# Optimization experiments

Measured on AMD Instinct MI355X. Metric: run time of the kernel, lower is better.

The kernel has to match this reference:

```python
import jax, jax.numpy as jnp
import numpy as np

B, N, F_IN, D = 32768, 4, 512, 64  # N fixed to 4 by the max_pool(4,1)+reshape


def setup_inputs() -> dict:
    key = jax.random.key(0)
    k1, k2, k3, k4 = jax.random.split(key, 4)
    scale = 1.0 / np.sqrt(F_IN)
    return {
        "drug": jax.random.normal(k1, (B, N, F_IN), dtype=jnp.float32),
        "Wk": jax.random.normal(k2, (F_IN, D), dtype=jnp.float32) * scale,
        "Wq": jax.random.normal(k3, (F_IN, D), dtype=jnp.float32) * scale,
        "Wv": jax.random.normal(k4, (F_IN, D), dtype=jnp.float32) * scale,
    }


def reference(drug, Wk, Wq, Wv):
    # projections: torch nn.Linear(bias=False) -> x @ W  (W stored as [in, out] here)
    k = jnp.einsum("bnf,fd->bnd", drug, Wk)
    q = jnp.einsum("bnf,fd->bnd", drug, Wq)
    v = jnp.einsum("bnf,fd->bnd", drug, Wv)
    # score = bmm(K, Q^T); NOTE: no 1/sqrt(d) scaling, matching the source
    score = jnp.einsum("bnd,bmd->bnm", k, q)  # [B, N, N]
    attn = jax.nn.softmax(score, axis=2)
    out = jnp.einsum("bnm,bmd->bnd", attn, v)  # [B, N, D]
    # max_pool2d kernel (4,1), stride (4,1) over N=4 -> max over axis 1, then reshape [B, D]
    return jnp.max(out, axis=1)
```

## Files before the change

### kernel.cpp

```cpp
#include <hip/hip_runtime.h>
#include <hip/hip_fp16.h>

#define BTOT   32768
#define FIN    512
#define NCOLS  192
#define KSTEPS 16
#define NTILES 12
#define WH_ELEMS (KSTEPS * NTILES * 64 * 8)
#define CHUNK_HALVES (NTILES * 64 * 8)
#define CHUNK_BYTES  (CHUNK_HALVES * 2)

using half8   = __attribute__((ext_vector_type(8))) _Float16;
using floatx4 = __attribute__((ext_vector_type(4))) float;

#define GLOAD_LDS16(gp, lp)                                                  \
    __builtin_amdgcn_global_load_lds(                                        \
        (const __attribute__((address_space(1))) void*)(gp),                 \
        (__attribute__((address_space(3))) void*)(lp), 16, 0, 0)

__global__ void convert_w_kernel(const float* __restrict__ Wk,
                                 const float* __restrict__ Wq,
                                 const float* __restrict__ Wv,
                                 _Float16* __restrict__ Wh) {
    int idx = blockIdx.x * blockDim.x + threadIdx.x;
    if (idx >= WH_ELEMS) return;
    int j    = idx & 7;
    int lane = (idx >> 3) & 63;
    int t    = (idx >> 9) % NTILES;
    int kk   = idx / CHUNK_HALVES;
    int k = kk * 32 + (lane >> 4) * 8 + j;
    int n = t * 16 + (lane & 15);
    const float* src = (n < 64) ? Wk : (n < 128) ? Wq : Wv;
    Wh[idx] = (_Float16)src[k * 64 + (n & 63)];
}

__global__ __launch_bounds__(256) void attn_fused_kernel(
        const float* __restrict__ drug,
        const _Float16* __restrict__ Wh,
        float* __restrict__ out)
{
    __shared__ __align__(16) char lds[2 * CHUNK_BYTES];

    const int tid  = threadIdx.x;
    const int wave = tid >> 6;
    const int lane = tid & 63;
    const int quad = lane >> 4;
    const int l15  = lane & 15;

    const int row = blockIdx.x * 64 + wave * 16 + l15;
    const float* arow = drug + (size_t)row * FIN + quad * 8;
    const char* gW = (const char*)Wh;

    floatx4 acc[NTILES];
#pragma unroll
    for (int t = 0; t < NTILES; ++t) acc[t] = (floatx4){0.f, 0.f, 0.f, 0.f};

#define STAGE(K)                                                             \
    do {                                                                     \
        const char* _s = gW + (size_t)(K) * CHUNK_BYTES;                     \
        char* _d = lds + ((K) & 1) * CHUNK_BYTES;                            \
        _Pragma("unroll")                                                    \
        for (int _i = 0; _i < 3; ++_i) {                                     \
            const int _off = (wave + 4 * _i) * 1024;                         \
            GLOAD_LDS16(_s + _off + lane * 16, _d + _off);                   \
        }                                                                    \
    } while (0)

    STAGE(0);
    float4 a0 = ((const float4*)arow)[0];
    float4 a1 = ((const float4*)arow)[1];
    STAGE(1);

#pragma unroll
    for (int k = 0; k < KSTEPS; ++k) {
        if (k < KSTEPS - 1)
            asm volatile("s_waitcnt vmcnt(3)" ::: "memory");
        else
            asm volatile("s_waitcnt vmcnt(0)" ::: "memory");
        asm volatile("" ::: "memory");
        __builtin_amdgcn_s_barrier();
        asm volatile("" ::: "memory");

        float4 n0, n1;
        if (k < KSTEPS - 1) {
            const float4* ap = (const float4*)(arow + (k + 1) * 32);
            n0 = ap[0];
            n1 = ap[1];
        }

        half8 af;
        af[0] = (_Float16)a0.x; af[1] = (_Float16)a0.y;
        af[2] = (_Float16)a0.z; af[3] = (_Float16)a0.w;
        af[4] = (_Float16)a1.x; af[5] = (_Float16)a1.y;
        af[6] = (_Float16)a1.z; af[7] = (_Float16)a1.w;

        const _Float16* lh = (const _Float16*)(lds + (k & 1) * CHUNK_BYTES);
#pragma unroll
        for (int t = 0; t < NTILES; ++t) {
            half8 bf = *((const half8*)(lh + (t * 64 + lane) * 8));
            acc[t] = __builtin_amdgcn_mfma_f32_16x16x32_f16(af, bf, acc[t], 0, 0, 0);
        }

        if (k < KSTEPS - 2) {
            asm volatile("" ::: "memory");
            __builtin_amdgcn_s_barrier();
            asm volatile("" ::: "memory");
            STAGE(k + 2);
        }
        a0 = n0; a1 = n1;
    }
#undef STAGE

    float p[4][4];
#pragma unroll
    for (int n = 0; n < 4; ++n)
#pragma unroll
        for (int m = 0; m < 4; ++m) {
            float s = 0.f;
#pragma unroll
            for (int t = 0; t < 4; ++t) s += acc[t][n] * acc[4 + t][m];
            p[n][m] = s;
        }

#pragma unroll
    for (int mask = 1; mask < 16; mask <<= 1) {
#pragma unroll
        for (int n = 0; n < 4; ++n)
#pragma unroll
            for (int m = 0; m < 4; ++m)
                p[n][m] += __shfl_xor(p[n][m], mask, 64);
    }

    float res[4] = {-INFINITY, -INFINITY, -INFINITY, -INFINITY};
#pragma unroll
    for (int n = 0; n < 4; ++n) {
        float mx = fmaxf(fmaxf(p[n][0], p[n][1]), fmaxf(p[n][2], p[n][3]));
        float e0 = __expf(p[n][0] - mx);
        float e1 = __expf(p[n][1] - mx);
        float e2 = __expf(p[n][2] - mx);
        float e3 = __expf(p[n][3] - mx);
        float inv = 1.f / (e0 + e1 + e2 + e3);
#pragma unroll
        for (int t = 0; t < 4; ++t) {
            float o = (e0 * acc[8 + t][0] + e1 * acc[8 + t][1] +
                       e2 * acc[8 + t][2] + e3 * acc[8 + t][3]) * inv;
            res[t] = fmaxf(res[t], o);
        }
    }

    const int b = blockIdx.x * 16 + wave * 4 + quad;
#pragma unroll
    for (int t = 0; t < 4; ++t)
        out[b * 64 + t * 16 + l15] = res[t];
}

extern "C" void kernel_launch(void* const* d_in, const int* in_sizes, int n_in,
                              void* d_out, int out_size, void* d_ws, size_t ws_size,
                              hipStream_t stream) {
    const float* drug = (const float*)d_in[0];
    const float* Wk   = (const float*)d_in[1];
    const float* Wq   = (const float*)d_in[2];
    const float* Wv   = (const float*)d_in[3];
    float* out = (float*)d_out;
    _Float16* Wh = (_Float16*)d_ws;

    convert_w_kernel<<<(WH_ELEMS + 255) / 256, 256, 0, stream>>>(Wk, Wq, Wv, Wh);
    attn_fused_kernel<<<BTOT / 16, 256, 0, stream>>>(drug, Wh, out);
}
```

Baseline: 372.0 us.

## Keep full K/Q weights resident in LDS, stream V from global, persistent row tiles

Splits the converted fp16 weights into a K/Q section and a separate V section. Each 512-thread block loads the whole K/Q weight matrix (128 KB) into LDS once, then loops over four 128-row tiles, so the per-k-step double-buffered staging and its barriers go away. V weight fragments are read straight from global/L2 into registers with a one-step prefetch. This cuts repeated weight staging and synchronisation, at the cost of large LDS use (one block per CU), fewer blocks, and extra register pressure from the prefetched V fragments.

After: 708.2 us. +90.4%, slower.

```diff
diff --git a/kernel.cpp b/kernel.cpp
--- a/kernel.cpp
+++ b/kernel.cpp
@@ -3,12 +3,16 @@
 
 #define BTOT   32768
 #define FIN    512
-#define NCOLS  192
 #define KSTEPS 16
 #define NTILES 12
 #define WH_ELEMS (KSTEPS * NTILES * 64 * 8)
 #define CHUNK_HALVES (NTILES * 64 * 8)
-#define CHUNK_BYTES  (CHUNK_HALVES * 2)
+#define KQ_HALVES (KSTEPS * 8 * 512)
+#define KQ_BYTES  (KQ_HALVES * 2)
+#define WAVES  8
+#define ROWTILES 4
+#define ROWS_PER_BLOCK (WAVES * 16 * ROWTILES)
+#define NBLOCKS (BTOT * 4 / ROWS_PER_BLOCK)
 
 using half8   = __attribute__((ext_vector_type(8))) _Float16;
 using floatx4 = __attribute__((ext_vector_type(4))) float;
@@ -31,15 +35,19 @@
     int k = kk * 32 + (lane >> 4) * 8 + j;
     int n = t * 16 + (lane & 15);
     const float* src = (n < 64) ? Wk : (n < 128) ? Wq : Wv;
-    Wh[idx] = (_Float16)src[k * 64 + (n & 63)];
+    _Float16 val = (_Float16)src[k * 64 + (n & 63)];
+    size_t dst = (t < 8)
+        ? ((size_t)(kk * 8 + t) * 512 + lane * 8 + j)
+        : (size_t)KQ_HALVES + ((size_t)(kk * 4 + (t - 8)) * 512 + lane * 8 + j);
+    Wh[dst] = val;
 }
 
-__global__ __launch_bounds__(256) void attn_fused_kernel(
+__global__ __launch_bounds__(512) void attn_fused_kernel(
         const float* __restrict__ drug,
         const _Float16* __restrict__ Wh,
         float* __restrict__ out)
 {
-    __shared__ __align__(16) char lds[2 * CHUNK_BYTES];
+    extern __shared__ __align__(16) char lds[];
 
     const int tid  = threadIdx.x;
     const int wave = tid >> 6;
@@ -47,111 +55,114 @@
     const int quad = lane >> 4;
     const int l15  = lane & 15;
 
-    const int row = blockIdx.x * 64 + wave * 16 + l15;
-    const float* arow = drug + (size_t)row * FIN + quad * 8;
-    const char* gW = (const char*)Wh;
+    {
+        const char* gk = (const char*)Wh;
+#pragma unroll
+        for (int i = 0; i < 16; ++i) {
+            const int off = i * 8192 + wave * 1024;
+            GLOAD_LDS16(gk + off + lane * 16, lds + off);
+        }
+    }
 
-    floatx4 acc[NTILES];
-#pragma unroll
-    for (int t = 0; t < NTILES; ++t) acc[t] = (floatx4){0.f, 0.f, 0.f, 0.f};
+    const half8* vf = (const half8*)(Wh + KQ_HALVES) + lane;
 
-#define STAGE(K)                                                             \
-    do {                                                                     \
-        const char* _s = gW + (size_t)(K) * CHUNK_BYTES;                     \
-        char* _d = lds + ((K) & 1) * CHUNK_BYTES;                            \
-        _Pragma("unroll")                                                    \
-        for (int _i = 0; _i < 3; ++_i) {                                     \
-            const int _off = (wave + 4 * _i) * 1024;                         \
-            GLOAD_LDS16(_s + _off + lane * 16, _d + _off);                   \
-        }                                                                    \
-    } while (0)
-
-    STAGE(0);
+    const int rowbase = blockIdx.x * ROWS_PER_BLOCK + wave * 16 + l15;
+    const float* arow = drug + (size_t)rowbase * FIN + quad * 8;
     float4 a0 = ((const float4*)arow)[0];
     float4 a1 = ((const float4*)arow)[1];
-    STAGE(1);
+    half8 v0 = vf[0], v1 = vf[64], v2 = vf[128], v3 = vf[192];
+
+    asm volatile("s_waitcnt vmcnt(0)" ::: "memory");
+    __builtin_amdgcn_s_barrier();
+
+    const int bbase = blockIdx.x * (ROWS_PER_BLOCK / 4) + wave * 4 + quad;
+
+#pragma unroll 1
+    for (int rt = 0; rt < ROWTILES; ++rt) {
+        floatx4 acc[NTILES];
+#pragma unroll
+        for (int t = 0; t < NTILES; ++t) acc[t] = (floatx4){0.f, 0.f, 0.f, 0.f};
+
+        const float* pfrow = (rt < ROWTILES - 1) ? arow + 128 * FIN : arow;
 
 #pragma unroll
-    for (int k = 0; k < KSTEPS; ++k) {
-        if (k < KSTEPS - 1)
-            asm volatile("s_waitcnt vmcnt(3)" ::: "memory");
-        else
-            asm volatile("s_waitcnt vmcnt(0)" ::: "memory");
-        asm volatile("" ::: "memory");
-        __builtin_amdgcn_s_barrier();
-        asm volatile("" ::: "memory");
+        for (int k = 0; k < KSTEPS; ++k) {
+            float4 n0, n1;
+            half8 w0, w1, w2, w3;
+            {
+                const float4* ap = (k < KSTEPS - 1)
+                    ? (const float4*)(arow + (k + 1) * 32)
+                    : (const float4*)pfrow;
+                n0 = ap[0];
+                n1 = ap[1];
+                const half8* vp = (k < KSTEPS - 1) ? vf + (k + 1) * 256 : vf;
+                w0 = vp[0]; w1 = vp[64]; w2 = vp[128]; w3 = vp[192];
+            }
 
-        float4 n0, n1;
-        if (k < KSTEPS - 1) {
-            const float4* ap = (const float4*)(arow + (k + 1) * 32);
-            n0 = ap[0];
-            n1 = ap[1];
+            half8 af;
+            af[0] = (_Float16)a0.x; af[1] = (_Float16)a0.y;
+            af[2] = (_Float16)a0.z; af[3] = (_Float16)a0.w;
+            af[4] = (_Float16)a1.x; af[5] = (_Float16)a1.y;
+            af[6] = (_Float16)a1.z; af[7] = (_Float16)a1.w;
+
+            const _Float16* lh = (const _Float16*)(lds + k * 8192);
+#pragma unroll
+            for (int t = 0; t < 8; ++t) {
+                half8 bf = *((const half8*)(lh + t * 512 + lane * 8));
+                acc[t] = __builtin_amdgcn_mfma_f32_16x16x32_f16(af, bf, acc[t], 0, 0, 0);
+            }
+            acc[8]  = __builtin_amdgcn_mfma_f32_16x16x32_f16(af, v0, acc[8],  0, 0, 0);
+            acc[9]  = __builtin_amdgcn_mfma_f32_16x16x32_f16(af, v1, acc[9],  0, 0, 0);
+            acc[10] = __builtin_amdgcn_mfma_f32_16x16x32_f16(af, v2, acc[10], 0, 0, 0);
+            acc[11] = __builtin_amdgcn_mfma_f32_16x16x32_f16(af, v3, acc[11], 0, 0, 0);
+
+            a0 = n0; a1 = n1;
+            v0 = w0; v1 = w1; v2 = w2; v3 = w3;
         }
+        arow += 128 * FIN;
 
-        half8 af;
-        af[0] = (_Float16)a0.x; af[1] = (_Float16)a0.y;
-        af[2] = (_Float16)a0.z; af[3] = (_Float16)a0.w;
-        af[4] = (_Float16)a1.x; af[5] = (_Float16)a1.y;
-        af[6] = (_Float16)a1.z; af[7] = (_Float16)a1.w;
-
-        const _Float16* lh = (const _Float16*)(lds + (k & 1) * CHUNK_BYTES);
-#pragma unroll
-        for (int t = 0; t < NTILES; ++t) {
-            half8 bf = *((const half8*)(lh + (t * 64 + lane) * 8));
-            acc[t] = __builtin_amdgcn_mfma_f32_16x16x32_f16(af, bf, acc[t], 0, 0, 0);
-        }
-
-        if (k < KSTEPS - 2) {
-            asm volatile("" ::: "memory");
-            __builtin_amdgcn_s_barrier();
-            asm volatile("" ::: "memory");
-            STAGE(k + 2);
-        }
-        a0 = n0; a1 = n1;
-    }
-#undef STAGE
-
-    float p[4][4];
-#pragma unroll
-    for (int n = 0; n < 4; ++n)
-#pragma unroll
-        for (int m = 0; m < 4; ++m) {
-            float s = 0.f;
-#pragma unroll
-            for (int t = 0; t < 4; ++t) s += acc[t][n] * acc[4 + t][m];
-            p[n][m] = s;
-        }
-
-#pragma unroll
-    for (int mask = 1; mask < 16; mask <<= 1) {
+        float p[4][4];
 #pragma unroll
         for (int n = 0; n < 4; ++n)
 #pragma unroll
-            for (int m = 0; m < 4; ++m)
-                p[n][m] += __shfl_xor(p[n][m], mask, 64);
+            for (int m = 0; m < 4; ++m) {
+                float s = 0.f;
+#pragma unroll
+                for (int t = 0; t < 4; ++t) s += acc[t][n] * acc[4 + t][m];
+                p[n][m] = s;
+            }
+
+#pragma unroll
+        for (int mask = 1; mask < 16; mask <<= 1) {
+#pragma unroll
+            for (int n = 0; n < 4; ++n)
+#pragma unroll
+                for (int m = 0; m < 4; ++m)
+                    p[n][m] += __shfl_xor(p[n][m], mask, 64);
+        }
+
+        float res[4] = {-INFINITY, -INFINITY, -INFINITY, -INFINITY};
+#pragma unroll
+        for (int n = 0; n < 4; ++n) {
+            float mx = fmaxf(fmaxf(p[n][0], p[n][1]), fmaxf(p[n][2], p[n][3]));
+            float e0 = __expf(p[n][0] - mx);
+            float e1 = __expf(p[n][1] - mx);
+            float e2 = __expf(p[n][2] - mx);
+            float e3 = __expf(p[n][3] - mx);
+            float inv = 1.f / (e0 + e1 + e2 + e3);
+#pragma unroll
+            for (int t = 0; t < 4; ++t) {
+                float o = (e0 * acc[8 + t][0] + e1 * acc[8 + t][1] +
+                           e2 * acc[8 + t][2] + e3 * acc[8 + t][3]) * inv;
+                res[t] = fmaxf(res[t], o);
+            }
+        }
+
+        const int b = bbase + rt * 32;
+#pragma unroll
+        for (int t = 0; t < 4; ++t)
+            out[b * 64 + t * 16 + l15] = res[t];
     }
-
-    float res[4] = {-INFINITY, -INFINITY, -INFINITY, -INFINITY};
-#pragma unroll
-    for (int n = 0; n < 4; ++n) {
-        float mx = fmaxf(fmaxf(p[n][0], p[n][1]), fmaxf(p[n][2], p[n][3]));
-        float e0 = __expf(p[n][0] - mx);
-        float e1 = __expf(p[n][1] - mx);
-        float e2 = __expf(p[n][2] - mx);
-        float e3 = __expf(p[n][3] - mx);
-        float inv = 1.f / (e0 + e1 + e2 + e3);
-#pragma unroll
-        for (int t = 0; t < 4; ++t) {
-            float o = (e0 * acc[8 + t][0] + e1 * acc[8 + t][1] +
-                       e2 * acc[8 + t][2] + e3 * acc[8 + t][3]) * inv;
-            res[t] = fmaxf(res[t], o);
-        }
-    }
-
-    const int b = blockIdx.x * 16 + wave * 4 + quad;
-#pragma unroll
-    for (int t = 0; t < 4; ++t)
-        out[b * 64 + t * 16 + l15] = res[t];
 }
 
 extern "C" void kernel_launch(void* const* d_in, const int* in_sizes, int n_in,
@@ -164,6 +175,13 @@
     float* out = (float*)d_out;
     _Float16* Wh = (_Float16*)d_ws;
 
+    static bool attr_set = false;
+    if (!attr_set) {
+        hipFuncSetAttribute((const void*)attn_fused_kernel,
+                            hipFuncAttributeMaxDynamicSharedMemorySize, KQ_BYTES);
+        attr_set = true;
+    }
+
     convert_w_kernel<<<(WH_ELEMS + 255) / 256, 256, 0, stream>>>(Wk, Wq, Wv, Wh);
-    attn_fused_kernel<<<BTOT / 16, 256, 0, stream>>>(drug, Wh, out);
+    attn_fused_kernel<<<NBLOCKS, 512, KQ_BYTES, stream>>>(drug, Wh, out);
 }
```
